# Performance work log

Hardware: AMD Instinct MI355X
Metric: run time of the kernel (lower is better)

## Reference

```python
import jax, jax.numpy as jnp
import numpy as np

B, C, W, H = 4, 64, 64, 64
CQK = C // 8  # query/key channels


def setup_inputs() -> dict:
    key = jax.random.key(0)
    ks = jax.random.split(key, 8)
    s = 0.05
    return {
        "x": jax.random.normal(ks[0], (B, C, W, H), jnp.float32),
        "Wq": jax.random.normal(ks[1], (CQK, C), jnp.float32) * s,
        "bq": jax.random.normal(ks[2], (CQK,), jnp.float32) * s,
        "Wk": jax.random.normal(ks[3], (CQK, C), jnp.float32) * s,
        "bk": jax.random.normal(ks[4], (CQK,), jnp.float32) * s,
        "Wv": jax.random.normal(ks[5], (C, C), jnp.float32) * s,
        "bv": jax.random.normal(ks[6], (C,), jnp.float32) * s,
        # torch init is zeros; use a nonzero value so the attention path is exercised
        "gamma": jax.random.normal(ks[7], (1,), jnp.float32) * s,
    }


def reference(x, Wq, bq, Wk, bk, Wv, bv, gamma):
    b, c, w, h = x.shape
    n = w * h
    xf = x.reshape(b, c, n)  # B, C, N
    # 1x1 convs == per-pixel linear maps
    q = jnp.einsum("oc,bcn->bno", Wq, xf) + bq           # B, N, Cqk
    k = jnp.einsum("oc,bcn->bon", Wk, xf) + bk[:, None]   # B, Cqk, N
    energy = jnp.einsum("bno,bom->bnm", q, k)             # B, N, N
    attn = jax.nn.softmax(energy, axis=-1)                # B, N, N
    v = jnp.einsum("oc,bcn->bon", Wv, xf) + bv[:, None]   # B, C, N
    # out[b,c,j] = sum_n v[b,c,n] * attn[j,n]  (bmm with attention^T)
    out = jnp.einsum("bcn,bjn->bcj", v, attn)
    out = out.reshape(b, c, w, h)
    return gamma * out + x
```

## Files before the change

kernel.cpp:

```cpp
#include <hip/hip_runtime.h>

typedef short s16x8 __attribute__((ext_vector_type(8)));
typedef float f32x4 __attribute__((ext_vector_type(4)));
typedef float f32x16 __attribute__((ext_vector_type(16)));
typedef unsigned u32x4 __attribute__((ext_vector_type(4)));

#define BB 4
#define NN 4096
#define LOG2E 1.4426950408889634f

__device__ __forceinline__ unsigned short f2bf(float f) {
    unsigned int u = __builtin_bit_cast(unsigned int, f);
    u += 0x7fff + ((u >> 16) & 1);
    return (unsigned short)(u >> 16);
}

__device__ __forceinline__ unsigned pk2(float lo, float hi) {
    return __builtin_amdgcn_perm(__builtin_bit_cast(unsigned, hi),
                                 __builtin_bit_cast(unsigned, lo), 0x07060302u);
}

__device__ __forceinline__ void pl32swap(unsigned &a, unsigned &b) {
    asm volatile("v_permlane32_swap_b32 %0, %1" : "+v"(a), "+v"(b));
}

__global__ __launch_bounds__(256) void proj_kernel(
    const float* __restrict__ x,
    const float* __restrict__ Wq, const float* __restrict__ bq,
    const float* __restrict__ Wk, const float* __restrict__ bk,
    const float* __restrict__ Wv, const float* __restrict__ bv,
    unsigned short* __restrict__ Qw, unsigned short* __restrict__ Kw,
    unsigned short* __restrict__ Vc)
{
    __shared__ __attribute__((aligned(16))) unsigned short sW[80 * 72];
    __shared__ __attribute__((aligned(16))) unsigned short xT[64 * 72];
    __shared__ float sb[80];

    int tid = threadIdx.x;
    int b  = blockIdx.x >> 6;
    int n0 = (blockIdx.x & 63) << 6;

    for (int i = tid; i < 1280; i += 256) {
        int o = i >> 4, c4 = (i & 15) << 2;
        const float* src = (o < 8) ? &Wq[o * 64 + c4]
                         : ((o < 16) ? &Wk[(o - 8) * 64 + c4]
                                     : &Wv[(o - 16) * 64 + c4]);
        float4 v = *(const float4*)src;
        float sc = (o < 8) ? LOG2E : 1.f;
        sW[o * 72 + c4 + 0] = f2bf(v.x * sc);
        sW[o * 72 + c4 + 1] = f2bf(v.y * sc);
        sW[o * 72 + c4 + 2] = f2bf(v.z * sc);
        sW[o * 72 + c4 + 3] = f2bf(v.w * sc);
    }
    if (tid < 80)
        sb[tid] = (tid < 8) ? bq[tid] * LOG2E
                            : ((tid < 16) ? bk[tid - 8] : bv[tid - 16]);
    for (int i = tid; i < 1024; i += 256) {
        int c = i >> 4, p4 = (i & 15) << 2;
        float4 v = *(const float4*)&x[(((size_t)b * 64 + c) << 12) + n0 + p4];
        xT[(p4 + 0) * 72 + c] = f2bf(v.x);
        xT[(p4 + 1) * 72 + c] = f2bf(v.y);
        xT[(p4 + 2) * 72 + c] = f2bf(v.z);
        xT[(p4 + 3) * 72 + c] = f2bf(v.w);
    }
    __syncthreads();

    int w = tid >> 6, l = tid & 63, g = l >> 4, q16 = l & 15;
    int pix = w * 16 + q16;

    s16x8 bf0 = *(const s16x8*)&xT[pix * 72 + g * 8];
    s16x8 bf1 = *(const s16x8*)&xT[pix * 72 + 32 + g * 8];

    s16x8 a0[5], a1[5];
#pragma unroll
    for (int ot = 0; ot < 5; ++ot) {
        a0[ot] = *(const s16x8*)&sW[(ot * 16 + q16) * 72 + g * 8];
        a1[ot] = *(const s16x8*)&sW[(ot * 16 + q16) * 72 + 32 + g * 8];
    }
    __syncthreads();

    unsigned short* sV = xT;
    size_t base16 = ((size_t)(b << 12) + n0 + pix) << 4;

#pragma unroll
    for (int ot = 0; ot < 5; ++ot) {
        f32x4 acc = {0.f, 0.f, 0.f, 0.f};
        acc = __builtin_amdgcn_mfma_f32_16x16x32_bf16(a0[ot], bf0, acc, 0, 0, 0);
        acc = __builtin_amdgcn_mfma_f32_16x16x32_bf16(a1[ot], bf1, acc, 0, 0, 0);
#pragma unroll
        for (int r = 0; r < 4; ++r) {
            int orow = ot * 16 + g * 4 + r;
            unsigned short hv = f2bf(acc[r] + sb[orow]);
            if (ot == 0) {
                if (orow < 8) {
                    Qw[base16 + orow] = hv;
                    Qw[base16 + orow + 8] = 0;
                } else {
                    Kw[base16 + orow - 8] = hv;
                    Kw[base16 + orow] = 0;
                }
            } else {
                sV[(orow - 16) * 72 + pix] = hv;
            }
        }
    }
    __syncthreads();

#pragma unroll
    for (int i = tid; i < 512; i += 256) {
        int jj = i >> 6, c = i & 63;
        u32x4 v = *(const u32x4*)&sV[c * 72 + jj * 8];
        int jglob = ((blockIdx.x & 63) << 3) + jj;
        *(u32x4*)&Vc[(((size_t)b * 512 + jglob) * 64 + c) * 8] = v;
    }
}

__global__ __launch_bounds__(1024) void attn_kernel(
    const unsigned short* __restrict__ Qw, const unsigned short* __restrict__ Kw,
    const unsigned short* __restrict__ Vc, const float* __restrict__ x,
    const float* __restrict__ gamma, float* __restrict__ outp)
{
    __shared__ __attribute__((aligned(16))) float sO[64 * 68];
    __shared__ float sL[8 * 64];
    __shared__ float sGL[64];

    int tid = threadIdx.x;
    int w = tid >> 6, l = tid & 63, r31 = l & 31, hi = l >> 5;
    int wq = w >> 3, wk = w & 7;
    int p = blockIdx.x;
    int xcd = p & 7, qgrp = p >> 3;
    int b = xcd >> 1;
    int n0 = ((qgrp << 1) | (xcd & 1)) << 6;
    float gm = gamma[0];

    s16x8 qf = *(const s16x8*)((const char*)Qw + ((size_t)b << 17)
                               + ((size_t)(n0 + wq * 32 + r31) << 5) + (hi << 4));
    const char* KbW = (const char*)Kw + ((size_t)b << 17) + (wk << 14)
                    + (r31 << 5) + (hi << 4);
    const char* VcB = (const char*)Vc + ((size_t)b << 19) + (wk << 16)
                    + (hi << 10) + (r31 << 4);

    f32x16 zz;
#pragma unroll
    for (int i = 0; i < 16; ++i) zz[i] = 0.f;

    f32x16 acc0, acc1;
#pragma unroll
    for (int i = 0; i < 16; ++i) { acc0[i] = 0.f; acc1[i] = 0.f; }
    float la = 0.f;

    s16x8 K_a, A0_a, A1_a, B0_a, B1_a;
    s16x8 K_b, A0_b, A1_b, B0_b, B1_b;

#define LOADSET(S, kp, vp) do {                                             \
        K_##S  = *(const s16x8*)(kp);                                       \
        A0_##S = *(const s16x8*)(vp);                                       \
        B0_##S = *(const s16x8*)((vp) + 512);                               \
        A1_##S = *(const s16x8*)((vp) + 2048);                              \
        B1_##S = *(const s16x8*)((vp) + 2560);                              \
    } while (0)

#define STEP(S) do {                                                        \
        f32x16 E = __builtin_amdgcn_mfma_f32_32x32x16_bf16(K_##S, qf, zz, 0, 0, 0); \
        _Pragma("unroll")                                                   \
        for (int i = 0; i < 16; ++i) E[i] = __builtin_amdgcn_exp2f(E[i]);   \
        la += (((E[0] + E[1]) + (E[2] + E[3])) + ((E[4] + E[5]) + (E[6] + E[7]))) \
            + (((E[8] + E[9]) + (E[10] + E[11])) + ((E[12] + E[13]) + (E[14] + E[15]))); \
        unsigned x0 = pk2(E[0], E[1]),   x1 = pk2(E[2], E[3]);              \
        unsigned x2 = pk2(E[4], E[5]),   x3 = pk2(E[6], E[7]);              \
        unsigned x4 = pk2(E[8], E[9]),   x5 = pk2(E[10], E[11]);            \
        unsigned x6 = pk2(E[12], E[13]), x7 = pk2(E[14], E[15]);            \
        pl32swap(x0, x2); pl32swap(x1, x3);                                 \
        pl32swap(x4, x6); pl32swap(x5, x7);                                 \
        u32x4 u0 = {x0, x1, x2, x3}, u1 = {x4, x5, x6, x7};                 \
        s16x8 pf0 = __builtin_bit_cast(s16x8, u0);                          \
        s16x8 pf1 = __builtin_bit_cast(s16x8, u1);                          \
        acc0 = __builtin_amdgcn_mfma_f32_32x32x16_bf16(A0_##S, pf0, acc0, 0, 0, 0); \
        acc0 = __builtin_amdgcn_mfma_f32_32x32x16_bf16(A1_##S, pf1, acc0, 0, 0, 0); \
        acc1 = __builtin_amdgcn_mfma_f32_32x32x16_bf16(B0_##S, pf0, acc1, 0, 0, 0); \
        acc1 = __builtin_amdgcn_mfma_f32_32x32x16_bf16(B1_##S, pf1, acc1, 0, 0, 0); \
    } while (0)

    const char* ka = KbW;
    const char* va = VcB;
    const char* kb = KbW + 1024;
    const char* vb = VcB + 4096;

    LOADSET(a, ka, va);
    LOADSET(b, kb, vb);

#pragma unroll 1
    for (int tt = 0; tt < 7; ++tt) {
        ka += 2048; va += 8192;
        STEP(a);
        LOADSET(a, ka, va);
        kb += 2048; vb += 8192;
        STEP(b);
        LOADSET(b, kb, vb);
    }
    STEP(a);
    STEP(b);

#undef LOADSET
#undef STEP

    la += __shfl_xor(la, 32);
    if (l < 32) sL[wk * 64 + wq * 32 + l] = la;

#pragma unroll
    for (int s = 0; s < 8; ++s) {
        __syncthreads();
#pragma unroll
        for (int B = 0; B < 8; ++B) {
            if (((wk + s) & 7) == B) {
                const int R2 = B & 3;
                float e0 = (B < 4) ? acc0[R2 * 4 + 0] : acc1[R2 * 4 + 0];
                float e1 = (B < 4) ? acc0[R2 * 4 + 1] : acc1[R2 * 4 + 1];
                float e2 = (B < 4) ? acc0[R2 * 4 + 2] : acc1[R2 * 4 + 2];
                float e3 = (B < 4) ? acc0[R2 * 4 + 3] : acc1[R2 * 4 + 3];
                float* pp = &sO[(B * 8 + hi * 4) * 68 + wq * 32 + r31];
                if (s == 0) {
                    pp[0] = e0; pp[68] = e1; pp[136] = e2; pp[204] = e3;
                } else {
                    pp[0] += e0; pp[68] += e1; pp[136] += e2; pp[204] += e3;
                }
            }
        }
    }
    __syncthreads();

    if (tid < 64) {
        float L = 0.f;
#pragma unroll
        for (int wk2 = 0; wk2 < 8; ++wk2) L += sL[wk2 * 64 + tid];
        sGL[tid] = gm / L;
    }
    __syncthreads();

#pragma unroll
    for (int pp = 0; pp < 4; ++pp) {
        int c = pp * 16 + w;
        size_t idx = (((size_t)b * 64 + c) << 12) + n0 + l;
        outp[idx] = sGL[l] * sO[c * 68 + l] + x[idx];
    }
}

extern "C" void kernel_launch(void* const* d_in, const int* in_sizes, int n_in,
                              void* d_out, int out_size, void* d_ws, size_t ws_size,
                              hipStream_t stream) {
    const float* x     = (const float*)d_in[0];
    const float* Wq    = (const float*)d_in[1];
    const float* bq    = (const float*)d_in[2];
    const float* Wk    = (const float*)d_in[3];
    const float* bk    = (const float*)d_in[4];
    const float* Wv    = (const float*)d_in[5];
    const float* bv    = (const float*)d_in[6];
    const float* gamma = (const float*)d_in[7];
    float* out = (float*)d_out;

    unsigned short* Qw = (unsigned short*)d_ws;
    unsigned short* Kw = Qw + (size_t)BB * NN * 16;
    unsigned short* Vc = Kw + (size_t)BB * NN * 16;

    proj_kernel<<<256, 256, 0, stream>>>(x, Wq, bq, Wk, bk, Wv, bv, Qw, Kw, Vc);
    attn_kernel<<<256, 1024, 0, stream>>>(Qw, Kw, Vc, x, gamma, out);
}
```

Measured before the change: 29.76 us.

## Fuse projection and attention kernels with a grid-wide atomic barrier

Merges the projection kernel and the attention kernel into one 1024-thread launch, using a global atomic counter as a grid barrier between the phases. The projection block-to-tile mapping is remapped to match the attention XCD layout. This removes the second kernel launch and the gap between kernels, but adds a hipMemsetAsync for the barrier and relies on all 256 blocks being co-resident. Only a quarter of the threads do the projection MFMA work, so that phase runs at lower occupancy.

```diff
diff --git a/kernel.cpp b/kernel.cpp
--- a/kernel.cpp
+++ b/kernel.cpp
@@ -24,23 +24,32 @@
     asm volatile("v_permlane32_swap_b32 %0, %1" : "+v"(a), "+v"(b));
 }
 
-__global__ __launch_bounds__(256) void proj_kernel(
+__global__ __launch_bounds__(1024) void fused_kernel(
     const float* __restrict__ x,
     const float* __restrict__ Wq, const float* __restrict__ bq,
     const float* __restrict__ Wk, const float* __restrict__ bk,
     const float* __restrict__ Wv, const float* __restrict__ bv,
+    const float* __restrict__ gamma,
     unsigned short* __restrict__ Qw, unsigned short* __restrict__ Kw,
-    unsigned short* __restrict__ Vc)
+    unsigned short* __restrict__ Vc,
+    float* __restrict__ outp, unsigned* __restrict__ bar)
 {
     __shared__ __attribute__((aligned(16))) unsigned short sW[80 * 72];
     __shared__ __attribute__((aligned(16))) unsigned short xT[64 * 72];
     __shared__ float sb[80];
+    __shared__ __attribute__((aligned(16))) float sO[64 * 68];
+    __shared__ float sL[8 * 64];
+    __shared__ float sGL[64];
 
     int tid = threadIdx.x;
-    int b  = blockIdx.x >> 6;
-    int n0 = (blockIdx.x & 63) << 6;
-
-    for (int i = tid; i < 1280; i += 256) {
+    int p   = blockIdx.x;
+    int xcd = p & 7;
+    int b   = xcd >> 1;
+    int nb  = ((p >> 3) << 1) | (xcd & 1);
+    int n0  = nb << 6;
+    float gm = gamma[0];
+
+    for (int i = tid; i < 1280; i += 1024) {
         int o = i >> 4, c4 = (i & 15) << 2;
         const float* src = (o < 8) ? &Wq[o * 64 + c4]
                          : ((o < 16) ? &Wk[(o - 8) * 64 + c4]
@@ -55,8 +64,8 @@
     if (tid < 80)
         sb[tid] = (tid < 8) ? bq[tid] * LOG2E
                             : ((tid < 16) ? bk[tid - 8] : bv[tid - 16]);
-    for (int i = tid; i < 1024; i += 256) {
-        int c = i >> 4, p4 = (i & 15) << 2;
+    if (tid < 1024) {
+        int c = tid >> 4, p4 = (tid & 15) << 2;
         float4 v = *(const float4*)&x[(((size_t)b * 64 + c) << 12) + n0 + p4];
         xT[(p4 + 0) * 72 + c] = f2bf(v.x);
         xT[(p4 + 1) * 72 + c] = f2bf(v.y);
@@ -65,73 +74,78 @@
     }
     __syncthreads();
 
-    int w = tid >> 6, l = tid & 63, g = l >> 4, q16 = l & 15;
-    int pix = w * 16 + q16;
-
-    s16x8 bf0 = *(const s16x8*)&xT[pix * 72 + g * 8];
-    s16x8 bf1 = *(const s16x8*)&xT[pix * 72 + 32 + g * 8];
-
-    s16x8 a0[5], a1[5];
-#pragma unroll
-    for (int ot = 0; ot < 5; ++ot) {
-        a0[ot] = *(const s16x8*)&sW[(ot * 16 + q16) * 72 + g * 8];
-        a1[ot] = *(const s16x8*)&sW[(ot * 16 + q16) * 72 + 32 + g * 8];
+    s16x8 bf0, bf1, a0[5], a1[5];
+    if (tid < 256) {
+        int g = (tid & 63) >> 4, q16 = tid & 15;
+        int pix = (tid >> 6) * 16 + q16;
+        bf0 = *(const s16x8*)&xT[pix * 72 + g * 8];
+        bf1 = *(const s16x8*)&xT[pix * 72 + 32 + g * 8];
+#pragma unroll
+        for (int ot = 0; ot < 5; ++ot) {
+            a0[ot] = *(const s16x8*)&sW[(ot * 16 + q16) * 72 + g * 8];
+            a1[ot] = *(const s16x8*)&sW[(ot * 16 + q16) * 72 + 32 + g * 8];
+        }
     }
     __syncthreads();
 
     unsigned short* sV = xT;
-    size_t base16 = ((size_t)(b << 12) + n0 + pix) << 4;
-
-#pragma unroll
-    for (int ot = 0; ot < 5; ++ot) {
-        f32x4 acc = {0.f, 0.f, 0.f, 0.f};
-        acc = __builtin_amdgcn_mfma_f32_16x16x32_bf16(a0[ot], bf0, acc, 0, 0, 0);
-        acc = __builtin_amdgcn_mfma_f32_16x16x32_bf16(a1[ot], bf1, acc, 0, 0, 0);
-#pragma unroll
-        for (int r = 0; r < 4; ++r) {
-            int orow = ot * 16 + g * 4 + r;
-            unsigned short hv = f2bf(acc[r] + sb[orow]);
-            if (ot == 0) {
-                if (orow < 8) {
-                    Qw[base16 + orow] = hv;
-                    Qw[base16 + orow + 8] = 0;
+    if (tid < 256) {
+        int g = (tid & 63) >> 4, q16 = tid & 15;
+        int pix = (tid >> 6) * 16 + q16;
+        size_t base16 = ((size_t)(b << 12) + n0 + pix) << 4;
+#pragma unroll
+        for (int ot = 0; ot < 5; ++ot) {
+            f32x4 acc = {0.f, 0.f, 0.f, 0.f};
+            acc = __builtin_amdgcn_mfma_f32_16x16x32_bf16(a0[ot], bf0, acc, 0, 0, 0);
+            acc = __builtin_amdgcn_mfma_f32_16x16x32_bf16(a1[ot], bf1, acc, 0, 0, 0);
+#pragma unroll
+            for (int r = 0; r < 4; ++r) {
+                int orow = ot * 16 + g * 4 + r;
+                unsigned short hv = f2bf(acc[r] + sb[orow]);
+                if (ot == 0) {
+                    if (orow < 8) {
+                        Qw[base16 + orow] = hv;
+                        Qw[base16 + orow + 8] = 0;
+                    } else {
+                        Kw[base16 + orow - 8] = hv;
+                        Kw[base16 + orow] = 0;
+                    }
                 } else {
-                    Kw[base16 + orow - 8] = hv;
-                    Kw[base16 + orow] = 0;
+                    sV[(orow - 16) * 72 + pix] = hv;
                 }
-            } else {
-                sV[(orow - 16) * 72 + pix] = hv;
             }
         }
     }
     __syncthreads();
 
-#pragma unroll
-    for (int i = tid; i < 512; i += 256) {
-        int jj = i >> 6, c = i & 63;
+    if (tid < 512) {
+        int jj = tid >> 6, c = tid & 63;
         u32x4 v = *(const u32x4*)&sV[c * 72 + jj * 8];
-        int jglob = ((blockIdx.x & 63) << 3) + jj;
+        int jglob = (nb << 3) + jj;
         *(u32x4*)&Vc[(((size_t)b * 512 + jglob) * 64 + c) * 8] = v;
     }
-}
-
-__global__ __launch_bounds__(1024) void attn_kernel(
-    const unsigned short* __restrict__ Qw, const unsigned short* __restrict__ Kw,
-    const unsigned short* __restrict__ Vc, const float* __restrict__ x,
-    const float* __restrict__ gamma, float* __restrict__ outp)
-{
-    __shared__ __attribute__((aligned(16))) float sO[64 * 68];
-    __shared__ float sL[8 * 64];
-    __shared__ float sGL[64];
-
-    int tid = threadIdx.x;
-    int w = tid >> 6, l = tid & 63, r31 = l & 31, hi = l >> 5;
-    int wq = w >> 3, wk = w & 7;
-    int p = blockIdx.x;
-    int xcd = p & 7, qgrp = p >> 3;
-    int b = xcd >> 1;
-    int n0 = ((qgrp << 1) | (xcd & 1)) << 6;
-    float gm = gamma[0];
+    __syncthreads();
+
+    if (tid == 0) {
+        __threadfence();
+        unsigned my = __hip_atomic_fetch_add(&bar[0], 1u, __ATOMIC_ACQ_REL,
+                                             __HIP_MEMORY_SCOPE_AGENT);
+        if (my == 255u) {
+            __hip_atomic_store(&bar[0], 0u, __ATOMIC_RELAXED,
+                               __HIP_MEMORY_SCOPE_AGENT);
+            __hip_atomic_store(&bar[1], 1u, __ATOMIC_RELEASE,
+                               __HIP_MEMORY_SCOPE_AGENT);
+        } else {
+            while (__hip_atomic_load(&bar[1], __ATOMIC_ACQUIRE,
+                                     __HIP_MEMORY_SCOPE_AGENT) == 0u)
+                __builtin_amdgcn_s_sleep(2);
+        }
+        __threadfence();
+    }
+    __syncthreads();
+
+    int w2 = tid >> 6, l = tid & 63, r31 = l & 31, hi = l >> 5;
+    int wq = w2 >> 3, wk = w2 & 7;
 
     s16x8 qf = *(const s16x8*)((const char*)Qw + ((size_t)b << 17)
                                + ((size_t)(n0 + wq * 32 + r31) << 5) + (hi << 4));
@@ -239,7 +253,7 @@
 
 #pragma unroll
     for (int pp = 0; pp < 4; ++pp) {
-        int c = pp * 16 + w;
+        int c = pp * 16 + w2;
         size_t idx = (((size_t)b * 64 + c) << 12) + n0 + l;
         outp[idx] = sGL[l] * sO[c * 68 + l] + x[idx];
     }
@@ -261,7 +275,9 @@
     unsigned short* Qw = (unsigned short*)d_ws;
     unsigned short* Kw = Qw + (size_t)BB * NN * 16;
     unsigned short* Vc = Kw + (size_t)BB * NN * 16;
-
-    proj_kernel<<<256, 256, 0, stream>>>(x, Wq, bq, Wk, bk, Wv, bv, Qw, Kw, Vc);
-    attn_kernel<<<256, 1024, 0, stream>>>(Qw, Kw, Vc, x, gamma, out);
-}
+    unsigned* bar = (unsigned*)((char*)d_ws + (size_t)(16 << 20));
+
+    hipMemsetAsync(bar, 0, 16, stream);
+    fused_kernel<<<256, 1024, 0, stream>>>(x, Wq, bq, Wk, bk, Wv, bv, gamma,
+                                           Qw, Kw, Vc, out, bar);
+}
```

Measured after the change: 65.91 us. 2.21x slower.
